# Kernel optimization log

Measured on AMD Instinct MI355X. Metric: run time of the kernel, lower is better.

The kernel has to match this reference:

```python
import jax, jax.numpy as jnp
import numpy as np

N_HEAD = 12

def setup_inputs() -> dict:
    key = jax.random.key(0)
    ks = jax.random.split(key, 5)
    B, T, C = 4, 2048, 768
    scale = 0.02
    return {
        "x": jax.random.normal(ks[0], (B, T, C), dtype=jnp.float32),
        "W_attn": jax.random.normal(ks[1], (C, 3 * C), dtype=jnp.float32) * scale,
        "b_attn": jax.random.normal(ks[2], (3 * C,), dtype=jnp.float32) * scale,
        "W_proj": jax.random.normal(ks[3], (C, C), dtype=jnp.float32) * scale,
        "b_proj": jax.random.normal(ks[4], (C,), dtype=jnp.float32) * scale,
    }

def reference(x, W_attn, b_attn, W_proj, b_proj):
    B, T, C = x.shape
    H = N_HEAD
    D = C // H  # head dim
    qkv = x @ W_attn + b_attn  # [B,T,3C]
    q, k, v = jnp.split(qkv, 3, axis=-1)
    # [B,H,T,D]
    q = q.reshape(B, T, H, D).transpose(0, 2, 1, 3)
    k = k.reshape(B, T, H, D).transpose(0, 2, 1, 3)
    v = v.reshape(B, T, H, D).transpose(0, 2, 1, 3)
    scores = jnp.einsum('bhqd,bhkd->bhqk', q, k) / jnp.sqrt(jnp.float32(D))
    causal = jnp.tril(jnp.ones((T, T), dtype=bool))
    scores = jnp.where(causal[None, None, :, :], scores, jnp.float32(-jnp.inf))
    attn = jax.nn.softmax(scores, axis=-1)
    out = jnp.einsum('bhqk,bhkd->bhqd', attn, v)  # [B,H,T,D]
    out = out.transpose(0, 2, 1, 3).reshape(B, T, C)
    return out @ W_proj + b_proj
```

## Files before the change

kernel.cpp:

```cpp
#include <hip/hip_runtime.h>

typedef float f32x4 __attribute__((ext_vector_type(4)));
typedef __bf16 bf16x8 __attribute__((ext_vector_type(8)));
typedef unsigned short u16x8 __attribute__((ext_vector_type(8)));
typedef unsigned short u16x4 __attribute__((ext_vector_type(4)));

#define MFMA16(a, b, c) __builtin_amdgcn_mfma_f32_16x16x32_bf16((a), (b), (c), 0, 0, 0)

__device__ __forceinline__ unsigned short f2bf(float f) {
    __bf16 h = (__bf16)f;
    union { __bf16 h; unsigned short u; } c; c.h = h;
    return c.u;
}

__device__ __forceinline__ void gload_lds16(const unsigned short* g, unsigned short* l) {
    __builtin_amdgcn_global_load_lds(
        (const __attribute__((address_space(1))) unsigned int*)g,
        (__attribute__((address_space(3))) unsigned int*)l, 16, 0, 0);
}

__global__ void k_convert_bf16(const float* __restrict__ in,
                               unsigned short* __restrict__ out, int n) {
    int i = (blockIdx.x * 256 + threadIdx.x) * 4;
    if (i + 3 < n) {
        float4 v = *reinterpret_cast<const float4*>(in + i);
        ushort4 o;
        o.x = f2bf(v.x); o.y = f2bf(v.y); o.z = f2bf(v.z); o.w = f2bf(v.w);
        *reinterpret_cast<ushort4*>(out + i) = o;
    }
}

__global__ void k_transpose_bf16(const float* __restrict__ in,
                                 unsigned short* __restrict__ out, int R, int C) {
    __shared__ unsigned short tile[32][33];
    int bx = blockIdx.x * 32;
    int by = blockIdx.y * 32;
    int tx = threadIdx.x;
    int ty = threadIdx.y;
    #pragma unroll
    for (int i = ty; i < 32; i += 8)
        tile[i][tx] = f2bf(in[(size_t)(by + i) * C + bx + tx]);
    __syncthreads();
    #pragma unroll
    for (int i = ty; i < 32; i += 8)
        out[(size_t)(bx + i) * R + by + tx] = tile[tx][i];
}

template<int EPI>
__global__ __launch_bounds__(512) void k_gemm_bt(
    const unsigned short* __restrict__ A,
    const unsigned short* __restrict__ Bt,
    const float* __restrict__ bias,
    unsigned short* __restrict__ Qo,
    unsigned short* __restrict__ Ko,
    unsigned short* __restrict__ Vto,
    float* __restrict__ Co,
    int K)
{
    __shared__ unsigned short SM[(256 + 128) * 64];
    unsigned short* As = SM;
    unsigned short* Bs = SM + 256 * 64;
    const int nwg = gridDim.x * gridDim.y;
    const int bid0 = blockIdx.y * gridDim.x + blockIdx.x;
    const int logical = (bid0 & 7) * (nwg >> 3) + (bid0 >> 3);
    const int bm = logical / gridDim.x;
    const int bn = logical % gridDim.x;
    const int tid = threadIdx.x;
    const int w = tid >> 6, l = tid & 63;
    const int wm = w >> 1, wn = w & 1;
    const int ln = l & 15, kb = l >> 4;

    f32x4 acc[4][4];
    #pragma unroll
    for (int i = 0; i < 4; ++i)
        #pragma unroll
        for (int j = 0; j < 4; ++j)
            #pragma unroll
            for (int r = 0; r < 4; ++r) acc[i][j][r] = 0.f;

    const unsigned short* Ab = A + (size_t)(bm * 256) * K;
    const unsigned short* Bb = Bt + (size_t)(bn * 128) * K;

    const int srow = tid >> 3;
    const int sslot = tid & 7;
    const int csw = (sslot ^ (srow & 7)) * 8;

    for (int k0 = 0; k0 < K; k0 += 64) {
        #pragma unroll
        for (int j = 0; j < 4; ++j) {
            const int r = j * 64 + srow;
            gload_lds16(&Ab[(size_t)r * K + k0 + csw], &As[r * 64 + sslot * 8]);
        }
        #pragma unroll
        for (int j = 0; j < 2; ++j) {
            const int r = j * 64 + srow;
            gload_lds16(&Bb[(size_t)r * K + k0 + csw], &Bs[r * 64 + sslot * 8]);
        }
        __syncthreads();
        #pragma unroll
        for (int kh = 0; kh < 2; ++kh) {
            bf16x8 af[4], bfr[4];
            #pragma unroll
            for (int mt = 0; mt < 4; ++mt) {
                const int row = wm * 64 + mt * 16 + ln;
                const int slot = ((kh << 2) | kb) ^ (row & 7);
                af[mt] = *reinterpret_cast<const bf16x8*>(&As[row * 64 + slot * 8]);
            }
            #pragma unroll
            for (int nt = 0; nt < 4; ++nt) {
                const int row = wn * 64 + nt * 16 + ln;
                const int slot = ((kh << 2) | kb) ^ (row & 7);
                bfr[nt] = *reinterpret_cast<const bf16x8*>(&Bs[row * 64 + slot * 8]);
            }
            #pragma unroll
            for (int mt = 0; mt < 4; ++mt)
                #pragma unroll
                for (int nt = 0; nt < 4; ++nt)
                    acc[mt][nt] = MFMA16(af[mt], bfr[nt], acc[mt][nt]);
        }
        __syncthreads();
    }

    const float SC = 0.1803368801111204f;

    if (EPI == 0 && bn >= 12) {
        unsigned short* Ts = SM;
        const int cl_w = wn * 64;
        #pragma unroll
        for (int hh2 = 0; hh2 < 2; ++hh2) {
            if ((wm >> 1) == hh2) {
                #pragma unroll
                for (int mt = 0; mt < 4; ++mt) {
                    #pragma unroll
                    for (int nt = 0; nt < 4; ++nt) {
                        const int cl = cl_w + nt * 16 + ln;
                        const float bv = bias[bn * 128 + cl];
                        #pragma unroll
                        for (int r = 0; r < 4; ++r) {
                            const int rl = (wm & 1) * 64 + mt * 16 + kb * 4 + r;
                            const int pos = cl * 128 + ((((rl >> 3) ^ (cl & 7)) << 3) | (rl & 7));
                            Ts[pos] = f2bf(acc[mt][nt][r] + bv);
                        }
                    }
                }
            }
            __syncthreads();
            {
                const int cl = tid >> 2;
                const int col = bn * 128 + cl;
                const int cc = col - 1536;
                const int hh = cc >> 6, dd = cc & 63;
                #pragma unroll
                for (int j8 = 0; j8 < 4; ++j8) {
                    const int rb = (tid & 3) * 4 + j8;
                    u16x8 val = *reinterpret_cast<const u16x8*>(&Ts[cl * 128 + ((rb ^ (cl & 7)) << 3)]);
                    const int tg = bm * 256 + hh2 * 128 + rb * 8;
                    const int bb = tg >> 11;
                    const int tloc = tg & 2047;
                    const int grp = tloc & ~31;
                    const int jj = (tloc >> 3) & 3;
                    const int tlo = grp + 8 * ((2 * jj) & 3) + 4 * (jj >> 1);
                    const int thi = grp + 8 * ((2 * jj + 1) & 3) + 4 * (jj >> 1);
                    unsigned short* basep = &Vto[((size_t)((bb * 12 + hh) * 64 + dd)) * 2048];
                    *reinterpret_cast<u16x4*>(basep + tlo) =
                        __builtin_shufflevector(val, val, 0, 1, 2, 3);
                    *reinterpret_cast<u16x4*>(basep + thi) =
                        __builtin_shufflevector(val, val, 4, 5, 6, 7);
                }
            }
            __syncthreads();
        }
        return;
    }

    #pragma unroll
    for (int mt = 0; mt < 4; ++mt) {
        #pragma unroll
        for (int nt = 0; nt < 4; ++nt) {
            const int col = bn * 128 + wn * 64 + nt * 16 + ln;
            #pragma unroll
            for (int r = 0; r < 4; ++r) {
                const int row = bm * 256 + wm * 64 + mt * 16 + kb * 4 + r;
                float v = acc[mt][nt][r] + bias[col];
                if (EPI == 0) {
                    int cc = col >= 768 ? col - 768 : col;
                    int h = cc >> 6, d = cc & 63;
                    int b = row >> 11, t = row & 2047;
                    if (col < 768)
                        Qo[((size_t)((b * 12 + h) * 2048 + t)) * 64 + d] = f2bf(v * SC);
                    else
                        Ko[((size_t)((b * 12 + h) * 2048 + t)) * 64 + d] = f2bf(v);
                } else {
                    Co[(size_t)row * 768 + col] = v;
                }
            }
        }
    }
}

__global__ __launch_bounds__(512) void k_attn(
    const unsigned short* __restrict__ Q,
    const unsigned short* __restrict__ Kk,
    const unsigned short* __restrict__ Vt,
    unsigned short* __restrict__ Oo)
{
    __shared__ unsigned short Ks[2][2][4096];
    __shared__ unsigned short Vs[2][2][4096];
    const int bid0 = blockIdx.x;
    const int xcd = bid0 & 7;
    const int loc = bid0 >> 3;
    const int qb = 15 - (loc / 6);
    const int bh = xcd * 6 + (loc % 6);
    const int tid = threadIdx.x;
    const int w = tid >> 6, l = tid & 63;
    const int g = w >> 2, wq = w & 3;
    const int ln = l & 15, kb = l >> 4;
    const int kbq = kb * 4;
    const int b = bh / 12, h = bh - b * 12;
    const int q0w = qb * 128 + wq * 32;

    const unsigned short* Qb = Q + (size_t)bh * 2048 * 64;
    const unsigned short* Kb = Kk + (size_t)bh * 2048 * 64;
    const unsigned short* Vb = Vt + (size_t)bh * 64 * 2048;

    bf16x8 qf[2][2];
    #pragma unroll
    for (int qn = 0; qn < 2; ++qn) {
        const unsigned short* qr = &Qb[(size_t)(q0w + qn * 16 + ln) * 64 + kb * 8];
        qf[qn][0] = *reinterpret_cast<const bf16x8*>(qr);
        qf[qn][1] = *reinterpret_cast<const bf16x8*>(qr + 32);
    }

    bf16x8 vones;
    #pragma unroll
    for (int e = 0; e < 8; ++e) vones[e] = (__bf16)1.0f;

    f32x4 oaccT[2][4];
    f32x4 den[2];
    #pragma unroll
    for (int qn = 0; qn < 2; ++qn) {
        #pragma unroll
        for (int r = 0; r < 4; ++r) den[qn][r] = 0.f;
        #pragma unroll
        for (int dt = 0; dt < 4; ++dt)
            #pragma unroll
            for (int r = 0; r < 4; ++r) oaccT[qn][dt][r] = 0.f;
    }

    const int srow = tid >> 3;
    const int sslot = tid & 7;
    const int csw = (sslot ^ (srow & 7)) * 8;
    const int nsuper = qb + 1;
    const int lastkt = (q0w + 31) >> 6;

    #define STAGE8(s_, buf_)                                                        \
        {                                                                           \
            _Pragma("unroll")                                                       \
            for (int c = 0; c < 2; ++c) {                                           \
                const int key0 = (s_) * 128 + c * 64;                               \
                gload_lds16(&Kb[(size_t)(key0 + srow) * 64 + csw],                  \
                            &Ks[buf_][c][srow * 64 + sslot * 8]);                   \
                gload_lds16(&Vb[(size_t)srow * 2048 + key0 + csw],                  \
                            &Vs[buf_][c][srow * 64 + sslot * 8]);                   \
            }                                                                       \
        }

    STAGE8(0, 0);
    __syncthreads();

    for (int s = 0; s < nsuper; ++s) {
        const int buf = s & 1;
        if (s + 1 < nsuper) STAGE8(s + 1, buf ^ 1);

        const int kt = 2 * s + g;
        if (kt <= lastkt) {
            const int kbase = kt * 64;
            const unsigned short* Ksb = &Ks[buf][g][0];
            const unsigned short* Vsb = &Vs[buf][g][0];
            bf16x8 kf[4][2];
            #pragma unroll
            for (int km = 0; km < 4; ++km) {
                const int row = km * 16 + ln;
                #pragma unroll
                for (int dh = 0; dh < 2; ++dh) {
                    const int slot = ((dh << 2) | kb) ^ (row & 7);
                    kf[km][dh] = *reinterpret_cast<const bf16x8*>(&Ksb[row * 64 + slot * 8]);
                }
            }
            f32x4 st[4][2];
            #pragma unroll
            for (int km = 0; km < 4; ++km)
                #pragma unroll
                for (int qn = 0; qn < 2; ++qn) {
                    #pragma unroll
                    for (int r = 0; r < 4; ++r) st[km][qn][r] = 0.f;
                    st[km][qn] = MFMA16(kf[km][0], qf[qn][0], st[km][qn]);
                    st[km][qn] = MFMA16(kf[km][1], qf[qn][1], st[km][qn]);
                }
            bf16x8 vf[4][2];
            #pragma unroll
            for (int dt = 0; dt < 4; ++dt) {
                const int row = dt * 16 + ln;
                #pragma unroll
                for (int kh = 0; kh < 2; ++kh) {
                    const int slot = ((kh << 2) | kb) ^ (row & 7);
                    vf[dt][kh] = *reinterpret_cast<const bf16x8*>(&Vsb[row * 64 + slot * 8]);
                }
            }

            const bool diag = (kt == lastkt);
            #pragma unroll
            for (int qn = 0; qn < 2; ++qn) {
                const int qrow = q0w + qn * 16 + ln;
                #pragma unroll
                for (int km = 0; km < 4; ++km) {
                    #pragma unroll
                    for (int r = 0; r < 4; ++r) {
                        float sv = st[km][qn][r];
                        if (diag) {
                            const int key = kbase + km * 16 + kbq + r;
                            sv = (key <= qrow) ? sv : -1e30f;
                        }
                        st[km][qn][r] = __builtin_amdgcn_exp2f(sv);
                    }
                }
            }
            bf16x8 pa[2][2];
            #pragma unroll
            for (int qn = 0; qn < 2; ++qn)
                #pragma unroll
                for (int kh = 0; kh < 2; ++kh) {
                    bf16x8 t;
                    #pragma unroll
                    for (int r = 0; r < 4; ++r) {
                        t[r]     = (__bf16)st[2 * kh][qn][r];
                        t[r + 4] = (__bf16)st[2 * kh + 1][qn][r];
                    }
                    pa[qn][kh] = t;
                }
            #pragma unroll
            for (int qn = 0; qn < 2; ++qn) {
                #pragma unroll
                for (int dt = 0; dt < 4; ++dt) {
                    oaccT[qn][dt] = MFMA16(pa[qn][0], vf[dt][0], oaccT[qn][dt]);
                    oaccT[qn][dt] = MFMA16(pa[qn][1], vf[dt][1], oaccT[qn][dt]);
                }
                den[qn] = MFMA16(pa[qn][0], vones, den[qn]);
                den[qn] = MFMA16(pa[qn][1], vones, den[qn]);
            }
        }
        __syncthreads();
    }

    float* OP = reinterpret_cast<float*>(&Ks[0][0][0]);
    float* DP = reinterpret_cast<float*>(&Vs[0][0][0]);
    if (g == 1) {
        #pragma unroll
        for (int qn = 0; qn < 2; ++qn) {
            #pragma unroll
            for (int dt = 0; dt < 4; ++dt)
                #pragma unroll
                for (int r = 0; r < 4; ++r)
                    OP[wq * 2048 + (qn * 16 + kbq + r) * 64 + dt * 16 + ln] = oaccT[qn][dt][r];
            if (ln == 0) {
                #pragma unroll
                for (int r = 0; r < 4; ++r)
                    DP[wq * 32 + qn * 16 + kbq + r] = den[qn][r];
            }
        }
    }
    __syncthreads();
    if (g == 0) {
        #pragma unroll
        for (int qn = 0; qn < 2; ++qn) {
            #pragma unroll
            for (int r = 0; r < 4; ++r) {
                float dsum = den[qn][r] + DP[wq * 32 + qn * 16 + kbq + r];
                const float inv = 1.0f / dsum;
                const int t = q0w + qn * 16 + kbq + r;
                #pragma unroll
                for (int dt = 0; dt < 4; ++dt) {
                    float num = oaccT[qn][dt][r] +
                                OP[wq * 2048 + (qn * 16 + kbq + r) * 64 + dt * 16 + ln];
                    Oo[((size_t)(b * 2048 + t)) * 768 + h * 64 + dt * 16 + ln] = f2bf(num * inv);
                }
            }
        }
    }
}

extern "C" void kernel_launch(void* const* d_in, const int* in_sizes, int n_in,
                              void* d_out, int out_size, void* d_ws, size_t ws_size,
                              hipStream_t stream) {
    const float* x      = (const float*)d_in[0];
    const float* W_attn = (const float*)d_in[1];
    const float* b_attn = (const float*)d_in[2];
    const float* W_proj = (const float*)d_in[3];
    const float* b_proj = (const float*)d_in[4];
    float* out = (float*)d_out;

    char* ws = (char*)d_ws;
    const size_t SZ_X  = (size_t)8192 * 768 * 2;
    const size_t SZ_WA = (size_t)2304 * 768 * 2;
    const size_t SZ_WP = (size_t)768 * 768 * 2;
    const size_t SZ_T  = (size_t)8192 * 768 * 2;

    unsigned short* x_bf = (unsigned short*)(ws);
    unsigned short* wa_t = (unsigned short*)(ws + SZ_X);
    unsigned short* wp_t = (unsigned short*)(ws + SZ_X + SZ_WA);
    unsigned short* Qb   = (unsigned short*)(ws + SZ_X + SZ_WA + SZ_WP);
    unsigned short* Kb   = (unsigned short*)(ws + SZ_X + SZ_WA + SZ_WP + SZ_T);
    unsigned short* Vtb  = (unsigned short*)(ws + SZ_X + SZ_WA + SZ_WP + 2 * SZ_T);
    unsigned short* attn_o = x_bf;

    k_convert_bf16<<<6144, 256, 0, stream>>>(x, x_bf, 8192 * 768);
    dim3 tb(32, 8);
    k_transpose_bf16<<<dim3(2304 / 32, 768 / 32), tb, 0, stream>>>(W_attn, wa_t, 768, 2304);
    k_transpose_bf16<<<dim3(768 / 32, 768 / 32), tb, 0, stream>>>(W_proj, wp_t, 768, 768);
    k_gemm_bt<0><<<dim3(18, 32), 512, 0, stream>>>(x_bf, wa_t, b_attn, Qb, Kb, Vtb, nullptr, 768);
    k_attn<<<768, 512, 0, stream>>>(Qb, Kb, Vtb, attn_o);
    k_gemm_bt<1><<<dim3(6, 32), 512, 0, stream>>>(attn_o, wp_t, b_proj, nullptr, nullptr, nullptr, out, 768);
}
```

Baseline: 135.4 us.

## Restructure attention to 4 waves with triple-buffered KV and no split-K merge

The attention kernel drops from 8 waves (two key-groups that split the key tiles, then merge partial results through LDS) to 4 waves that each walk every key tile sequentially. K/V staging becomes a 3-deep ring of 64-key tiles, prefetched two ahead and guarded by explicit vmcnt waits and s_barrier, which removes the per-iteration __syncthreads and the final LDS reduction. MFMA sections are wrapped in s_setprio to favour matrix issue. This trades intra-block key parallelism for less synchronisation and merge overhead. It risks lower latency hiding, since each block now has half as many waves and a longer serial loop.

```diff
diff --git a/kernel.cpp b/kernel.cpp
--- a/kernel.cpp
+++ b/kernel.cpp
@@ -198,14 +198,14 @@
     }
 }
 
-__global__ __launch_bounds__(512) void k_attn(
+__global__ __launch_bounds__(256) void k_attn(
     const unsigned short* __restrict__ Q,
     const unsigned short* __restrict__ Kk,
     const unsigned short* __restrict__ Vt,
     unsigned short* __restrict__ Oo)
 {
-    __shared__ unsigned short Ks[2][2][4096];
-    __shared__ unsigned short Vs[2][2][4096];
+    __shared__ unsigned short Ks[3][64 * 64];
+    __shared__ unsigned short Vs[3][64 * 64];
     const int bid0 = blockIdx.x;
     const int xcd = bid0 & 7;
     const int loc = bid0 >> 3;
@@ -213,11 +213,10 @@
     const int bh = xcd * 6 + (loc % 6);
     const int tid = threadIdx.x;
     const int w = tid >> 6, l = tid & 63;
-    const int g = w >> 2, wq = w & 3;
     const int ln = l & 15, kb = l >> 4;
     const int kbq = kb * 4;
     const int b = bh / 12, h = bh - b * 12;
-    const int q0w = qb * 128 + wq * 32;
+    const int q0w = qb * 128 + w * 32;
 
     const unsigned short* Qb = Q + (size_t)bh * 2048 * 64;
     const unsigned short* Kb = Kk + (size_t)bh * 2048 * 64;
@@ -250,33 +249,43 @@
     const int srow = tid >> 3;
     const int sslot = tid & 7;
     const int csw = (sslot ^ (srow & 7)) * 8;
-    const int nsuper = qb + 1;
+    const int ntile = 2 * qb + 2;
     const int lastkt = (q0w + 31) >> 6;
 
-    #define STAGE8(s_, buf_)                                                        \
+    #define STAGE(kt_, buf_)                                                        \
         {                                                                           \
+            const int kb_ = (kt_) * 64;                                             \
             _Pragma("unroll")                                                       \
-            for (int c = 0; c < 2; ++c) {                                           \
-                const int key0 = (s_) * 128 + c * 64;                               \
-                gload_lds16(&Kb[(size_t)(key0 + srow) * 64 + csw],                  \
-                            &Ks[buf_][c][srow * 64 + sslot * 8]);                   \
-                gload_lds16(&Vb[(size_t)srow * 2048 + key0 + csw],                  \
-                            &Vs[buf_][c][srow * 64 + sslot * 8]);                   \
+            for (int j = 0; j < 2; ++j) {                                           \
+                const int r = j * 32 + srow;                                        \
+                gload_lds16(&Kb[(size_t)(kb_ + r) * 64 + csw],                      \
+                            &Ks[buf_][r * 64 + sslot * 8]);                         \
+                gload_lds16(&Vb[(size_t)r * 2048 + kb_ + csw],                      \
+                            &Vs[buf_][r * 64 + sslot * 8]);                         \
             }                                                                       \
         }
 
-    STAGE8(0, 0);
-    __syncthreads();
-
-    for (int s = 0; s < nsuper; ++s) {
-        const int buf = s & 1;
-        if (s + 1 < nsuper) STAGE8(s + 1, buf ^ 1);
-
-        const int kt = 2 * s + g;
+    STAGE(0, 0);
+    STAGE(1, 1);
+
+    for (int kt = 0; kt < ntile; ++kt) {
+        const int buf = kt % 3;
+        if (kt + 1 < ntile) {
+            asm volatile("s_waitcnt vmcnt(4)" ::: "memory");
+        } else {
+            asm volatile("s_waitcnt vmcnt(0)" ::: "memory");
+        }
+        __builtin_amdgcn_sched_barrier(0);
+        __builtin_amdgcn_s_barrier();
+        if (kt + 2 < ntile) {
+            const int nb3 = (kt + 2) % 3;
+            STAGE(kt + 2, nb3);
+        }
+
         if (kt <= lastkt) {
             const int kbase = kt * 64;
-            const unsigned short* Ksb = &Ks[buf][g][0];
-            const unsigned short* Vsb = &Vs[buf][g][0];
+            const unsigned short* Ksb = &Ks[buf][0];
+            const unsigned short* Vsb = &Vs[buf][0];
             bf16x8 kf[4][2];
             #pragma unroll
             for (int km = 0; km < 4; ++km) {
@@ -288,6 +297,7 @@
                 }
             }
             f32x4 st[4][2];
+            __builtin_amdgcn_s_setprio(1);
             #pragma unroll
             for (int km = 0; km < 4; ++km)
                 #pragma unroll
@@ -297,6 +307,7 @@
                     st[km][qn] = MFMA16(kf[km][0], qf[qn][0], st[km][qn]);
                     st[km][qn] = MFMA16(kf[km][1], qf[qn][1], st[km][qn]);
                 }
+            __builtin_amdgcn_s_setprio(0);
             bf16x8 vf[4][2];
             #pragma unroll
             for (int dt = 0; dt < 4; ++dt) {
@@ -338,6 +349,7 @@
                     }
                     pa[qn][kh] = t;
                 }
+            __builtin_amdgcn_s_setprio(1);
             #pragma unroll
             for (int qn = 0; qn < 2; ++qn) {
                 #pragma unroll
@@ -348,43 +360,20 @@
                 den[qn] = MFMA16(pa[qn][0], vones, den[qn]);
                 den[qn] = MFMA16(pa[qn][1], vones, den[qn]);
             }
-        }
-        __syncthreads();
-    }
-
-    float* OP = reinterpret_cast<float*>(&Ks[0][0][0]);
-    float* DP = reinterpret_cast<float*>(&Vs[0][0][0]);
-    if (g == 1) {
-        #pragma unroll
-        for (int qn = 0; qn < 2; ++qn) {
+            __builtin_amdgcn_s_setprio(0);
+        }
+    }
+
+    #pragma unroll
+    for (int qn = 0; qn < 2; ++qn) {
+        #pragma unroll
+        for (int r = 0; r < 4; ++r) {
+            const float inv = 1.0f / den[qn][r];
+            const int t = q0w + qn * 16 + kbq + r;
             #pragma unroll
             for (int dt = 0; dt < 4; ++dt)
-                #pragma unroll
-                for (int r = 0; r < 4; ++r)
-                    OP[wq * 2048 + (qn * 16 + kbq + r) * 64 + dt * 16 + ln] = oaccT[qn][dt][r];
-            if (ln == 0) {
-                #pragma unroll
-                for (int r = 0; r < 4; ++r)
-                    DP[wq * 32 + qn * 16 + kbq + r] = den[qn][r];
-            }
-        }
-    }
-    __syncthreads();
-    if (g == 0) {
-        #pragma unroll
-        for (int qn = 0; qn < 2; ++qn) {
-            #pragma unroll
-            for (int r = 0; r < 4; ++r) {
-                float dsum = den[qn][r] + DP[wq * 32 + qn * 16 + kbq + r];
-                const float inv = 1.0f / dsum;
-                const int t = q0w + qn * 16 + kbq + r;
-                #pragma unroll
-                for (int dt = 0; dt < 4; ++dt) {
-                    float num = oaccT[qn][dt][r] +
-                                OP[wq * 2048 + (qn * 16 + kbq + r) * 64 + dt * 16 + ln];
-                    Oo[((size_t)(b * 2048 + t)) * 768 + h * 64 + dt * 16 + ln] = f2bf(num * inv);
-                }
-            }
+                Oo[((size_t)(b * 2048 + t)) * 768 + h * 64 + dt * 16 + ln] =
+                    f2bf(oaccT[qn][dt][r] * inv);
         }
     }
 }
@@ -418,6 +407,6 @@
     k_transpose_bf16<<<dim3(2304 / 32, 768 / 32), tb, 0, stream>>>(W_attn, wa_t, 768, 2304);
     k_transpose_bf16<<<dim3(768 / 32, 768 / 32), tb, 0, stream>>>(W_proj, wp_t, 768, 768);
     k_gemm_bt<0><<<dim3(18, 32), 512, 0, stream>>>(x_bf, wa_t, b_attn, Qb, Kb, Vtb, nullptr, 768);
-    k_attn<<<768, 512, 0, stream>>>(Qb, Kb, Vtb, attn_o);
+    k_attn<<<768, 256, 0, stream>>>(Qb, Kb, Vtb, attn_o);
     k_gemm_bt<1><<<dim3(6, 32), 512, 0, stream>>>(attn_o, wp_t, b_proj, nullptr, nullptr, nullptr, out, 768);
 }
```

After: 138.2 us. 2.1% more time.
